# Kernel optimization log

Hardware: AMD Instinct MI355X
Metric: run time of the kernel (lower is better)

The kernel has to match this reference:

```python
import jax, jax.numpy as jnp
import numpy as np

K_SECTIONS = 8


def _make_sos(K=K_SECTIONS, seed=0):
    """Build K stable biquad sections [K, 6] = [b0,b1,b2,a0,a1,a2], unit DC gain."""
    rng = np.random.default_rng(seed)
    r_p = rng.uniform(0.5, 0.95, K)
    th_p = rng.uniform(0.1, 3.0, K)
    r_z = rng.uniform(0.5, 0.99, K)
    th_z = rng.uniform(0.1, 3.0, K)
    a1 = -2.0 * r_p * np.cos(th_p)
    a2 = r_p ** 2
    b1 = -2.0 * r_z * np.cos(th_z)
    b2 = r_z ** 2
    b0 = np.ones(K)
    g = (1.0 + a1 + a2) / (b0 + b1 + b2)  # normalize DC gain to 1 per section
    sos = np.stack([b0 * g, b1 * g, b2 * g, np.ones(K), a1, a2], axis=1)
    return jnp.asarray(sos, dtype=jnp.float32)


def setup_inputs() -> dict:
    key = jax.random.key(0)
    x = jax.random.normal(key, (128, 65536), dtype=jnp.float32)  # [C, T]
    return {"x": x, "sos": _make_sos()}


def reference(x, sos):
    """Fused SOS cascade: sequential direct-form-I biquad recurrence over time."""
    K = sos.shape[0]
    a0 = sos[:, 3]
    b0, b1, b2 = sos[:, 0] / a0, sos[:, 1] / a0, sos[:, 2] / a0  # [K]
    a1, a2 = sos[:, 4] / a0, sos[:, 5] / a0                      # [K]
    C, T = x.shape

    def step(carry, xt):  # xt: [C]
        x1, x2, y1, y2 = carry  # each [K, C]
        s = xt
        nx1, nx2, ny1, ny2 = [], [], [], []
        for k in range(K):  # fixed small unroll over cascaded sections
            y = (b0[k] * s + b1[k] * x1[k] + b2[k] * x2[k]
                 - a1[k] * y1[k] - a2[k] * y2[k])
            nx2.append(x1[k]); nx1.append(s)
            ny2.append(y1[k]); ny1.append(y)
            s = y
        carry = (jnp.stack(nx1), jnp.stack(nx2), jnp.stack(ny1), jnp.stack(ny2))
        return carry, s

    init = tuple(jnp.zeros((K, C), x.dtype) for _ in range(4))
    _, y = jax.lax.scan(step, init, x.T)  # scan over time axis -> y: [T, C]
    return y.T
```

## Files before the change

### kernel.cpp

```cpp
#include <hip/hip_runtime.h>


#define T_LEN   65536
#define NCH     128
#define CG      16
#define TB      1024
#define NTAP    144
#define HALO    128
#define XSPAN   (HALO + TB + 32)
#define XSTRIDE 1192
#define NQ4     (CG * (XSPAN / 4))
#define TPB     256

typedef _Float16 half8 __attribute__((ext_vector_type(8)));
typedef _Float16 half4h __attribute__((ext_vector_type(4)));
typedef float    f32x4 __attribute__((ext_vector_type(4)));

__global__ __launch_bounds__(TPB)
void FusedSOSCascade_20040317403806_kernel(const float* __restrict__ x,
                                           const float* __restrict__ sos,
                                           float* __restrict__ out) {
  __shared__ alignas(16) _Float16 lds_x[CG * XSTRIDE];
  __shared__ alignas(16) float hsA[8][160];
  __shared__ alignas(16) float hsB[4][160];

  const int tid = threadIdx.x;
  const int cg  = blockIdx.x & 7;
  const int tb  = blockIdx.x >> 3;
  const int c0  = cg * CG;
  const int t0  = tb * TB;

  if (tid < 8) {
    const int k = tid;
    const float a0 = sos[k * 6 + 3];
    const float b0 =  sos[k * 6 + 0] / a0;
    const float b1 =  sos[k * 6 + 1] / a0;
    const float b2 =  sos[k * 6 + 2] / a0;
    const float a1 =  sos[k * 6 + 4] / a0;
    const float a2 =  sos[k * 6 + 5] / a0;
    float h1 = 0.f, h2 = 0.f;
#pragma unroll 1
    for (int n = 0; n < NTAP; ++n) {
      float v = fmaf(-a1, h1, -a2 * h2);
      if (n == 0) v += b0;
      else if (n == 1) v += b1;
      else if (n == 2) v += b2;
      hsA[k][n] = v;
      h2 = h1; h1 = v;
    }
  } else if (tid >= 64) {
    const int st = tid - 64;
#pragma unroll 1
    for (int k0 = 0; k0 < 25; k0 += 5) {
      float4 v[5];
      int   row[5], col4[5];
#pragma unroll
      for (int j = 0; j < 5; ++j) {
        const int idx = st + (k0 + j) * 192;
        row[j]  = idx / (XSPAN / 4);
        col4[j] = idx - row[j] * (XSPAN / 4);
        float4 t = make_float4(0.f, 0.f, 0.f, 0.f);
        if (idx < NQ4) {
          const int gt = t0 - HALO + 4 * col4[j];
          if (gt >= 0 && gt < T_LEN)
            t = *(const float4*)(x + (size_t)(c0 + row[j]) * T_LEN + gt);
        }
        v[j] = t;
      }
#pragma unroll
      for (int j = 0; j < 5; ++j) {
        const int idx = st + (k0 + j) * 192;
        if (idx < NQ4) {
          half4h hv = { (_Float16)v[j].x, (_Float16)v[j].y,
                        (_Float16)v[j].z, (_Float16)v[j].w };
          *(half4h*)(&lds_x[row[j] * XSTRIDE + 4 * col4[j]]) = hv;
        }
      }
    }
  }
  __syncthreads();

#pragma unroll 1
  for (int idx = tid; idx < 4 * NTAP; idx += TPB) {
    const int p = idx / NTAP, t = idx - p * NTAP;
    const float* a = hsA[2 * p];
    const float* b = hsA[2 * p + 1];
    float s = 0.f;
    for (int i = 0; i <= t; ++i) s = fmaf(a[i], b[t - i], s);
    hsB[p][t] = s;
  }
  __syncthreads();
#pragma unroll 1
  for (int idx = tid; idx < 2 * NTAP; idx += TPB) {
    const int p = idx / NTAP, t = idx - p * NTAP;
    const float* a = hsB[2 * p];
    const float* b = hsB[2 * p + 1];
    float s = 0.f;
    for (int i = 0; i <= t; ++i) s = fmaf(a[i], b[t - i], s);
    hsA[p][t] = s;
  }
  __syncthreads();
#pragma unroll 1
  for (int t = tid; t < NTAP; t += TPB) {
    const float* a = hsA[0];
    const float* b = hsA[1];
    float s = 0.f;
    for (int i = 0; i <= t; ++i) s = fmaf(a[i], b[t - i], s);
    hsB[0][t] = s;
  }
  __syncthreads();

  const int wv = tid >> 6;
  const int l  = tid & 63;
  const int r  = l & 15;
  const int g  = l >> 4;

  half8 afrag[5];
#pragma unroll
  for (int m = 0; m < 5; ++m) {
    half8 af;
#pragma unroll
    for (int e = 0; e < 8; ++e) {
      const int i = r + 128 - 32 * m - 8 * g - e;
      const float hv = (i >= 0 && i < NTAP) ? hsB[0][i] : 0.f;
      af[e] = (_Float16)hv;
    }
    afrag[m] = af;
  }

  float* orow = out + (size_t)(c0 + r) * T_LEN + t0;
#pragma unroll 1
  for (int q = 0; q < 16; ++q) {
    const int tt = wv * 16 + q;
    f32x4 acc = {0.f, 0.f, 0.f, 0.f};
#pragma unroll
    for (int m = 0; m < 5; ++m) {
      const half8 bfrag =
          *(const half8*)(&lds_x[r * XSTRIDE + 16 * tt + 32 * m + 8 * g]);
      acc = __builtin_amdgcn_mfma_f32_16x16x32_f16(afrag[m], bfrag, acc,
                                                   0, 0, 0);
    }
    *(float4*)(orow + 16 * tt + 4 * g) =
        make_float4(acc[0], acc[1], acc[2], acc[3]);
  }
}

extern "C" void kernel_launch(void* const* d_in, const int* in_sizes, int n_in,
                              void* d_out, int out_size, void* d_ws, size_t ws_size,
                              hipStream_t stream) {
  const float* x   = (const float*)d_in[0];
  const float* sos = (const float*)d_in[1];
  float* out = (float*)d_out;
  (void)in_sizes; (void)n_in; (void)out_size; (void)d_ws; (void)ws_size;

  FusedSOSCascade_20040317403806_kernel<<<dim3(512), dim3(TPB), 0, stream>>>(
      x, sos, out);
}
```

Baseline: 104.8 us.

## Compute cascade impulse response via DPP pipeline and double block threads

Replaces the per-section impulse responses plus three rounds of shared-memory convolutions with a single wavefront pipeline. Lane k runs section k, and DPP row shifts pass each section's output to the next, which yields the cascaded impulse response directly and removes three barriers and the O(N^2) convolution work. The block grows from 256 to 512 threads, so the staging loads and the MFMA time tiles are spread over twice as many waves. Larger blocks may reduce how many blocks fit per CU.

```diff
diff --git a/kernel.cpp b/kernel.cpp
--- a/kernel.cpp
+++ b/kernel.cpp
@@ -2,7 +2,6 @@
 
 
 #define T_LEN   65536
-#define NCH     128
 #define CG      16
 #define TB      1024
 #define NTAP    144
@@ -10,19 +9,20 @@
 #define XSPAN   (HALO + TB + 32)
 #define XSTRIDE 1192
 #define NQ4     (CG * (XSPAN / 4))
-#define TPB     256
+#define Q4ROW   (XSPAN / 4)
+#define TPB     512
+#define NSTAGE  (TPB - 64)
 
-typedef _Float16 half8 __attribute__((ext_vector_type(8)));
+typedef _Float16 half8  __attribute__((ext_vector_type(8)));
 typedef _Float16 half4h __attribute__((ext_vector_type(4)));
-typedef float    f32x4 __attribute__((ext_vector_type(4)));
+typedef float    f32x4  __attribute__((ext_vector_type(4)));
 
 __global__ __launch_bounds__(TPB)
 void FusedSOSCascade_20040317403806_kernel(const float* __restrict__ x,
                                            const float* __restrict__ sos,
                                            float* __restrict__ out) {
   __shared__ alignas(16) _Float16 lds_x[CG * XSTRIDE];
-  __shared__ alignas(16) float hsA[8][160];
-  __shared__ alignas(16) float hsB[4][160];
+  __shared__ alignas(16) float hs[NTAP];
 
   const int tid = threadIdx.x;
   const int cg  = blockIdx.x & 7;
@@ -30,83 +30,61 @@
   const int c0  = cg * CG;
   const int t0  = tb * TB;
 
-  if (tid < 8) {
-    const int k = tid;
-    const float a0 = sos[k * 6 + 3];
-    const float b0 =  sos[k * 6 + 0] / a0;
-    const float b1 =  sos[k * 6 + 1] / a0;
-    const float b2 =  sos[k * 6 + 2] / a0;
-    const float a1 =  sos[k * 6 + 4] / a0;
-    const float a2 =  sos[k * 6 + 5] / a0;
-    float h1 = 0.f, h2 = 0.f;
-#pragma unroll 1
-    for (int n = 0; n < NTAP; ++n) {
-      float v = fmaf(-a1, h1, -a2 * h2);
-      if (n == 0) v += b0;
-      else if (n == 1) v += b1;
-      else if (n == 2) v += b2;
-      hsA[k][n] = v;
-      h2 = h1; h1 = v;
+  if (tid < 64) {
+    const int k = tid & 7;
+    const float a0  = sos[k * 6 + 3];
+    const float cb0 =  sos[k * 6 + 0] / a0;
+    const float cb1 =  sos[k * 6 + 1] / a0;
+    const float cb2 =  sos[k * 6 + 2] / a0;
+    const float cn1 = -(sos[k * 6 + 4] / a0);
+    const float cn2 = -(sos[k * 6 + 5] / a0);
+    float y = 0.f, z1 = 0.f, z2 = 0.f;
+#pragma unroll 4
+    for (int n = 0; n < NTAP + 7; ++n) {
+      const int ui = __builtin_amdgcn_update_dpp(0, __float_as_int(y),
+                                                 0x111, 0xf, 0xf, true);
+      float s = __int_as_float(ui);
+      if (tid == 0) s = (n == 0) ? 1.f : 0.f;
+      y  = fmaf(cb0, s, z1);
+      z1 = fmaf(cb1, s, fmaf(cn1, y, z2));
+      z2 = fmaf(cb2, s, cn2 * y);
+      if (tid == 7 && n >= 7) hs[n - 7] = y;
     }
-  } else if (tid >= 64) {
+  } else {
     const int st = tid - 64;
 #pragma unroll 1
-    for (int k0 = 0; k0 < 25; k0 += 5) {
-      float4 v[5];
-      int   row[5], col4[5];
+    for (int k0 = 0; k0 < 11; k0 += 6) {
+      float4 v[6];
+      const int kn = (k0 == 0) ? 6 : 5;
 #pragma unroll
-      for (int j = 0; j < 5; ++j) {
-        const int idx = st + (k0 + j) * 192;
-        row[j]  = idx / (XSPAN / 4);
-        col4[j] = idx - row[j] * (XSPAN / 4);
-        float4 t = make_float4(0.f, 0.f, 0.f, 0.f);
-        if (idx < NQ4) {
-          const int gt = t0 - HALO + 4 * col4[j];
-          if (gt >= 0 && gt < T_LEN)
-            t = *(const float4*)(x + (size_t)(c0 + row[j]) * T_LEN + gt);
+      for (int j = 0; j < 6; ++j) {
+        if (j < kn) {
+          const int idx = st + (k0 + j) * NSTAGE;
+          float4 t = make_float4(0.f, 0.f, 0.f, 0.f);
+          if (idx < NQ4) {
+            const int row = idx / Q4ROW;
+            const int c4  = idx - row * Q4ROW;
+            const int gt  = t0 - HALO + 4 * c4;
+            if (gt >= 0 && gt < T_LEN)
+              t = *(const float4*)(x + (size_t)(c0 + row) * T_LEN + gt);
+          }
+          v[j] = t;
         }
-        v[j] = t;
       }
 #pragma unroll
-      for (int j = 0; j < 5; ++j) {
-        const int idx = st + (k0 + j) * 192;
-        if (idx < NQ4) {
-          half4h hv = { (_Float16)v[j].x, (_Float16)v[j].y,
-                        (_Float16)v[j].z, (_Float16)v[j].w };
-          *(half4h*)(&lds_x[row[j] * XSTRIDE + 4 * col4[j]]) = hv;
+      for (int j = 0; j < 6; ++j) {
+        if (j < kn) {
+          const int idx = st + (k0 + j) * NSTAGE;
+          if (idx < NQ4) {
+            const int row = idx / Q4ROW;
+            const int c4  = idx - row * Q4ROW;
+            half4h hv = { (_Float16)v[j].x, (_Float16)v[j].y,
+                          (_Float16)v[j].z, (_Float16)v[j].w };
+            *(half4h*)(&lds_x[row * XSTRIDE + 4 * c4]) = hv;
+          }
         }
       }
     }
-  }
-  __syncthreads();
-
-#pragma unroll 1
-  for (int idx = tid; idx < 4 * NTAP; idx += TPB) {
-    const int p = idx / NTAP, t = idx - p * NTAP;
-    const float* a = hsA[2 * p];
-    const float* b = hsA[2 * p + 1];
-    float s = 0.f;
-    for (int i = 0; i <= t; ++i) s = fmaf(a[i], b[t - i], s);
-    hsB[p][t] = s;
-  }
-  __syncthreads();
-#pragma unroll 1
-  for (int idx = tid; idx < 2 * NTAP; idx += TPB) {
-    const int p = idx / NTAP, t = idx - p * NTAP;
-    const float* a = hsB[2 * p];
-    const float* b = hsB[2 * p + 1];
-    float s = 0.f;
-    for (int i = 0; i <= t; ++i) s = fmaf(a[i], b[t - i], s);
-    hsA[p][t] = s;
-  }
-  __syncthreads();
-#pragma unroll 1
-  for (int t = tid; t < NTAP; t += TPB) {
-    const float* a = hsA[0];
-    const float* b = hsA[1];
-    float s = 0.f;
-    for (int i = 0; i <= t; ++i) s = fmaf(a[i], b[t - i], s);
-    hsB[0][t] = s;
   }
   __syncthreads();
 
@@ -122,7 +100,7 @@
 #pragma unroll
     for (int e = 0; e < 8; ++e) {
       const int i = r + 128 - 32 * m - 8 * g - e;
-      const float hv = (i >= 0 && i < NTAP) ? hsB[0][i] : 0.f;
+      const float hv = (i >= 0 && i < NTAP) ? hs[i] : 0.f;
       af[e] = (_Float16)hv;
     }
     afrag[m] = af;
@@ -130,8 +108,8 @@
 
   float* orow = out + (size_t)(c0 + r) * T_LEN + t0;
 #pragma unroll 1
-  for (int q = 0; q < 16; ++q) {
-    const int tt = wv * 16 + q;
+  for (int q = 0; q < 8; ++q) {
+    const int tt = wv * 8 + q;
     f32x4 acc = {0.f, 0.f, 0.f, 0.f};
 #pragma unroll
     for (int m = 0; m < 5; ++m) {
```

Result: faster. 87.47 us (-16.5%).
